# Kernel tuning notes

Hardware: AMD Instinct MI355X
Metric: run time of the kernel (lower is better)

Reference implementation:

```python
import jax, jax.numpy as jnp
import numpy as np

WS = 7          # window size
HN = 6          # heads
C = 192         # emb dim
SHIFT = WS >> 1
L = WS * WS


def _rel_index(ws):
    c = np.stack(np.meshgrid(np.arange(ws), np.arange(ws), indexing='ij'), -1).reshape(-1, 2)
    d = c[:, None, :] - c[None, :, :] + (ws - 1)
    return jnp.asarray(d[..., 0] * (2 * ws - 1) + d[..., 1])  # (L, L) int


def _shift_mask(ws, shift):
    # after intra-window roll by -shift, positions >= ws-shift are wrapped pixels
    r = (np.arange(ws) >= ws - shift).astype(np.int32)
    rid = (2 * r[:, None] + r[None, :]).reshape(-1)  # (L,) region id
    m = np.where(rid[:, None] != rid[None, :], -100.0, 0.0).astype(np.float32)
    return jnp.asarray(m)  # (L, L)


def _ln(x, g, b, eps=1e-5):
    m = jnp.mean(x, -1, keepdims=True)
    v = jnp.mean(jnp.square(x - m), -1, keepdims=True)
    return (x - m) * jax.lax.rsqrt(v + eps) * g + b


def _wmsa(x, qkv_w, qkv_b, proj_w, proj_b, bias_table, rel_idx, mask):
    N, wn, Lx, Cx = x.shape
    dh = Cx // HN
    qkv = x @ qkv_w + qkv_b                      # (N, wn, L, 3C)
    q, k, v = jnp.split(qkv, 3, axis=-1)
    q = q.reshape(N, wn, Lx, HN, dh) * (dh ** -0.5)
    k = k.reshape(N, wn, Lx, HN, dh)
    v = v.reshape(N, wn, Lx, HN, dh)
    a = jnp.einsum('nwqhd,nwkhd->nwhqk', q, k)   # (N, wn, H, L, L)
    a = a + jnp.transpose(bias_table[rel_idx], (2, 0, 1))  # (H, L, L) bias
    if mask is not None:
        a = a + mask                             # (L, L) broadcast
    a = jax.nn.softmax(a, axis=-1)
    o = jnp.einsum('nwhqk,nwkhd->nwqhd', a, v).reshape(N, wn, Lx, Cx)
    return o @ proj_w + proj_b


def _layer(X, g1, b1, g2, b2, qkv_w, qkv_b, proj_w, proj_b, bias_table, rel_idx,
           w1, bb1, w2, bb2, mask):
    tmp = _ln(X, g1, b1)
    tmp = _wmsa(tmp, qkv_w, qkv_b, proj_w, proj_b, bias_table, rel_idx, mask)
    X = _ln(X + tmp, g2, b2)  # drop_path is identity in eval
    h = jax.nn.gelu(X @ w1 + bb1, approximate=False)
    return X + (h @ w2 + bb2)


def setup_inputs() -> dict:
    key = jax.random.key(0)
    ks = jax.random.split(key, 16)
    N, wn = 8, 1024
    s = 0.02
    d = {}
    d['X'] = jax.random.normal(ks[0], (N, wn, L, C), jnp.float32)
    d['ln1_g'] = jnp.ones((C,), jnp.float32)
    d['ln1_b'] = jnp.zeros((C,), jnp.float32)
    d['ln2_g'] = jnp.ones((C,), jnp.float32)
    d['ln2_b'] = jnp.zeros((C,), jnp.float32)
    d['win_qkv_w'] = jax.random.normal(ks[1], (C, 3 * C), jnp.float32) * s
    d['win_qkv_b'] = jnp.zeros((3 * C,), jnp.float32)
    d['win_proj_w'] = jax.random.normal(ks[2], (C, C), jnp.float32) * s
    d['win_proj_b'] = jnp.zeros((C,), jnp.float32)
    d['win_bias'] = jax.random.normal(ks[3], ((2 * WS - 1) ** 2, HN), jnp.float32) * s
    d['swin_qkv_w'] = jax.random.normal(ks[4], (C, 3 * C), jnp.float32) * s
    d['swin_qkv_b'] = jnp.zeros((3 * C,), jnp.float32)
    d['swin_proj_w'] = jax.random.normal(ks[5], (C, C), jnp.float32) * s
    d['swin_proj_b'] = jnp.zeros((C,), jnp.float32)
    d['swin_bias'] = jax.random.normal(ks[6], ((2 * WS - 1) ** 2, HN), jnp.float32) * s
    d['mlp_w1'] = jax.random.normal(ks[7], (C, 4 * C), jnp.float32) * s
    d['mlp_b1'] = jnp.zeros((4 * C,), jnp.float32)
    d['mlp_w2'] = jax.random.normal(ks[8], (4 * C, C), jnp.float32) * s
    d['mlp_b2'] = jnp.zeros((C,), jnp.float32)
    return d


def reference(X, ln1_g, ln1_b, ln2_g, ln2_b,
              win_qkv_w, win_qkv_b, win_proj_w, win_proj_b, win_bias,
              swin_qkv_w, swin_qkv_b, swin_proj_w, swin_proj_b, swin_bias,
              mlp_w1, mlp_b1, mlp_w2, mlp_b2):
    rel_idx = _rel_index(WS)
    mask = _shift_mask(WS, SHIFT)
    N, wn = X.shape[0], X.shape[1]
    # block 1: plain window MSA
    X = _layer(X, ln1_g, ln1_b, ln2_g, ln2_b, win_qkv_w, win_qkv_b, win_proj_w,
               win_proj_b, win_bias, rel_idx, mlp_w1, mlp_b1, mlp_w2, mlp_b2, None)
    # intra-window cyclic shift (torch dims (-2,-3) = W,H axes)
    X = X.reshape(N, wn, WS, WS, C)
    X = jnp.roll(X, (-SHIFT, -SHIFT), axis=(3, 2))
    X = X.reshape(N, wn, L, C)
    # block 2: shifted window MSA with mask
    X = _layer(X, ln1_g, ln1_b, ln2_g, ln2_b, swin_qkv_w, swin_qkv_b, swin_proj_w,
               swin_proj_b, swin_bias, rel_idx, mlp_w1, mlp_b1, mlp_w2, mlp_b2, mask)
    # reverse roll — repo uses dims (-1,-2) = (C, W) axes; replicated faithfully
    X = X.reshape(N, wn, WS, WS, C)
    X = jnp.roll(X, (SHIFT, SHIFT), axis=(4, 3))
    return X.reshape(N, wn, L, C)
```

## Files before the change

kernel.cpp:

```cpp
#include <hip/hip_runtime.h>
#include <hip/hip_bf16.h>
#include <math.h>

#define NTOK 401408
#define NWIN 8192

typedef __attribute__((ext_vector_type(8))) short bf16x8_t;
typedef __attribute__((ext_vector_type(4))) float f32x4_t;

__device__ __forceinline__ float bf2f(unsigned int u) {
    return __uint_as_float(u << 16);
}
__device__ __forceinline__ unsigned short f2bf(float f) {
    unsigned int x = __float_as_uint(f);
    x += 0x7fffu + ((x >> 16) & 1u);
    return (unsigned short)(x >> 16);
}
__device__ __forceinline__ unsigned int pack2bf(float a, float b) {
    return (unsigned int)f2bf(a) | ((unsigned int)f2bf(b) << 16);
}

__global__ void wt_all_kernel(const float* __restrict__ s0, const float* __restrict__ s1,
                              const float* __restrict__ s2, const float* __restrict__ s3,
                              const float* __restrict__ s4, const float* __restrict__ s5,
                              unsigned short* __restrict__ d0, unsigned short* __restrict__ d1,
                              unsigned short* __restrict__ d2, unsigned short* __restrict__ d3,
                              unsigned short* __restrict__ d4, unsigned short* __restrict__ d5) {
    int seg = blockIdx.y;
    const float* W; unsigned short* WT; int K, N;
    switch (seg) {
        case 0:  W = s0; WT = d0; K = 192; N = 576; break;
        case 1:  W = s1; WT = d1; K = 192; N = 576; break;
        case 2:  W = s2; WT = d2; K = 192; N = 192; break;
        case 3:  W = s3; WT = d3; K = 192; N = 192; break;
        case 4:  W = s4; WT = d4; K = 192; N = 768; break;
        default: W = s5; WT = d5; K = 768; N = 192; break;
    }
    int i = blockIdx.x * 256 + threadIdx.x;
    if (i >= N * K) return;
    int n = i / K, k = i - n * K;
    WT[i] = f2bf(W[(size_t)k * N + n]);
}

__global__ void bias_kernel(const float* __restrict__ bt0, const float* __restrict__ bt1,
                            float* __restrict__ bm) {
    int idx = blockIdx.x * 256 + threadIdx.x;
    int variant = blockIdx.y;
    const float* bt = variant ? bt1 : bt0;
    int r = idx & 3, lane = (idx >> 2) & 63, ni = (idx >> 8) & 3, mi = (idx >> 10) & 3, h = idx >> 12;
    int g = lane >> 4;
    int q = ni * 16 + (lane & 15);
    int k = mi * 16 + g * 4 + r;
    float v = 0.f;
    if (q < 49 && k < 49) {
        int qh = q / 7, qw = q - qh * 7, kh = k / 7, kw = k - kh * 7;
        v = bt[((qh - kh + 6) * 13 + (qw - kw + 6)) * 6 + h];
        if (variant) {
            int rq = 2 * (qh >= 4) + (qw >= 4), rk = 2 * (kh >= 4) + (kw >= 4);
            if (rq != rk) v -= 100.f;
        }
    }
    bm[(size_t)variant * 24576 + idx] = v;
}

template<int IN_BF16, int ROLL>
__global__ __launch_bounds__(256) void ln_kernel(const void* __restrict__ in,
                                                 unsigned short* __restrict__ out,
                                                 const float* __restrict__ g,
                                                 const float* __restrict__ b) {
    int tok  = blockIdx.x * 4 + (threadIdx.x >> 6);
    int lane = threadIdx.x & 63;
    int src = tok;
    if (ROLL) {
        int win = tok / 49, p2 = tok - win * 49;
        int h = p2 / 7, w = p2 - h * 7;
        int h2 = h + 3; if (h2 >= 7) h2 -= 7;
        int w2 = w + 3; if (w2 >= 7) w2 -= 7;
        src = win * 49 + h2 * 7 + w2;
    }
    float x0, x1, x2;
    if (IN_BF16) {
        const unsigned short* p = (const unsigned short*)in + (size_t)src * 192;
        x0 = bf2f(p[lane]); x1 = bf2f(p[lane + 64]); x2 = bf2f(p[lane + 128]);
    } else {
        const float* p = (const float*)in + (size_t)src * 192;
        x0 = p[lane]; x1 = p[lane + 64]; x2 = p[lane + 128];
    }
    float s  = x0 + x1 + x2;
    float sq = x0 * x0 + x1 * x1 + x2 * x2;
    for (int o = 32; o; o >>= 1) { s += __shfl_xor(s, o); sq += __shfl_xor(sq, o); }
    float m   = s * (1.f / 192.f);
    float var = sq * (1.f / 192.f) - m * m;
    float r   = rsqrtf(var + 1e-5f);
    unsigned short* q = out + (size_t)tok * 192;
    q[lane]       = f2bf((x0 - m) * r * g[lane]       + b[lane]);
    q[lane + 64]  = f2bf((x1 - m) * r * g[lane + 64]  + b[lane + 64]);
    q[lane + 128] = f2bf((x2 - m) * r * g[lane + 128] + b[lane + 128]);
}

#define EP_QKV        0
#define EP_PROJ1      1
#define EP_PROJ2      2
#define EP_MLP1       3
#define EP_MLP2_TRUNK 4
#define EP_MLP2_OUT   5

template<int NDIM, int KDIM, int NY, int EP>
__global__ __launch_bounds__(256) void gemm_kernel(const unsigned short* __restrict__ A,
                                                   const unsigned short* __restrict__ WT,
                                                   const float* __restrict__ bias,
                                                   const void* __restrict__ res,
                                                   void* __restrict__ out) {
    __shared__ __align__(16) unsigned short As[2][128][40];
    __shared__ __align__(16) unsigned short Bs[2][96][40];
    int tid = threadIdx.x;
    int nwg = gridDim.x;
    int id = blockIdx.x;
    int id2 = (id & 7) * (nwg >> 3) + (id >> 3);
    int by = id2 % NY, bx = id2 / NY;
    int rowBase = bx * 128;
    int colBase = by * 96;

    int cr = tid >> 2, cp = (tid & 3) * 8;
    const unsigned short* Ab = A  + (size_t)rowBase * KDIM + cp;
    const unsigned short* Bb = WT + (size_t)colBase * KDIM + cp;

    uint4 a0, a1, b0, b1;
    const int NT = KDIM / 32;

    #define LOADK(k0)                                                          \
        do {                                                                   \
            a0 = *(const uint4*)(Ab + (size_t)cr * KDIM + (k0));               \
            a1 = *(const uint4*)(Ab + (size_t)(cr + 64) * KDIM + (k0));        \
            b0 = *(const uint4*)(Bb + (size_t)cr * KDIM + (k0));               \
            if (tid < 128) b1 = *(const uint4*)(Bb + (size_t)(cr + 64) * KDIM + (k0)); \
        } while (0)
    #define WRITEK(buf)                                                        \
        do {                                                                   \
            *(uint4*)&As[buf][cr][cp] = a0;                                    \
            *(uint4*)&As[buf][cr + 64][cp] = a1;                               \
            *(uint4*)&Bs[buf][cr][cp] = b0;                                    \
            if (tid < 128) *(uint4*)&Bs[buf][cr + 64][cp] = b1;                \
        } while (0)

    LOADK(0);
    WRITEK(0);

    int wave = tid >> 6, lane = tid & 63;
    int wm = wave >> 1, wn = wave & 1;
    int kq = lane >> 4, lr = lane & 15;

    f32x4_t acc[4][3] = {};
    for (int kt = 0; kt < NT; ++kt) {
        if (kt + 1 < NT) LOADK((kt + 1) * 32);
        __syncthreads();
        int buf = kt & 1;
        bf16x8_t afr[4], bfr[3];
        #pragma unroll
        for (int mi = 0; mi < 4; ++mi)
            afr[mi] = *(const bf16x8_t*)&As[buf][wm * 64 + mi * 16 + lr][kq * 8];
        #pragma unroll
        for (int ni = 0; ni < 3; ++ni)
            bfr[ni] = *(const bf16x8_t*)&Bs[buf][wn * 48 + ni * 16 + lr][kq * 8];
        #pragma unroll
        for (int mi = 0; mi < 4; ++mi)
            #pragma unroll
            for (int ni = 0; ni < 3; ++ni)
                acc[mi][ni] = __builtin_amdgcn_mfma_f32_16x16x32_bf16(
                    afr[mi], bfr[ni], acc[mi][ni], 0, 0, 0);
        if (kt + 1 < NT) WRITEK((kt + 1) & 1);
    }
    #undef LOADK
    #undef WRITEK

    const float* resf = (const float*)res;
    const unsigned short* resb = (const unsigned short*)res;
    #pragma unroll
    for (int mi = 0; mi < 4; ++mi) {
        #pragma unroll
        for (int ni = 0; ni < 3; ++ni) {
            int col = colBase + wn * 48 + ni * 16 + lr;
            float bcol = bias[col];
            #pragma unroll
            for (int r = 0; r < 4; ++r) {
                int rloc = rowBase + wm * 64 + mi * 16 + kq * 4 + r;
                float v = acc[mi][ni][r] + bcol;
                if (EP == EP_QKV) {
                    if (colBase < 192) v *= 0.17677669529663687f;
                    ((unsigned short*)out)[(size_t)rloc * NDIM + col] = f2bf(v);
                } else if (EP == EP_PROJ1) {
                    v += resf[(size_t)rloc * 192 + col];
                    ((unsigned short*)out)[(size_t)rloc * 192 + col] = f2bf(v);
                } else if (EP == EP_PROJ2) {
                    int win = rloc / 49, p2 = rloc - win * 49;
                    int h = p2 / 7, w = p2 - h * 7;
                    int h2 = h + 3; if (h2 >= 7) h2 -= 7;
                    int w2 = w + 3; if (w2 >= 7) w2 -= 7;
                    v += resf[((size_t)win * 49 + h2 * 7 + w2) * 192 + col];
                    ((unsigned short*)out)[(size_t)rloc * 192 + col] = f2bf(v);
                } else if (EP == EP_MLP1) {
                    float gl = 0.5f * v * (1.f + erff(v * 0.70710678118654752f));
                    ((unsigned short*)out)[(size_t)rloc * NDIM + col] = f2bf(gl);
                } else if (EP == EP_MLP2_TRUNK) {
                    v += bf2f((unsigned int)resb[(size_t)rloc * 192 + col]);
                    ((float*)out)[(size_t)rloc * 192 + col] = v;
                } else {
                    v += bf2f((unsigned int)resb[(size_t)rloc * 192 + col]);
                    int win = rloc / 49, p2 = rloc - win * 49;
                    int h = p2 / 7, w = p2 - h * 7;
                    int w2 = w + 3; if (w2 >= 7) w2 -= 7;
                    int c2 = col + 3; if (c2 >= 192) c2 -= 192;
                    ((float*)out)[((size_t)win * 49 + h * 7 + w2) * 192 + c2] = v;
                }
            }
        }
    }
}

__global__ __launch_bounds__(64) void attn_kernel(const unsigned short* __restrict__ qkv,
                                                  const float* __restrict__ bm,
                                                  unsigned short* __restrict__ outp) {
    __shared__ unsigned short P[64][72];
    __shared__ unsigned short VT[32][72];
    int head = blockIdx.x, wloc = blockIdx.y;
    int lane = threadIdx.x;
    int g = lane >> 4, lr = lane & 15;
    const unsigned short* base = qkv + (size_t)wloc * 49 * 576;

    for (int i = lane; i < 256; i += 64) {
        int tok = i >> 2, seg = i & 3;
        uint4 u = make_uint4(0u, 0u, 0u, 0u);
        if (tok < 49)
            u = *(const uint4*)(base + (size_t)tok * 576 + 384 + head * 32 + seg * 8);
        const unsigned short* us = (const unsigned short*)&u;
        #pragma unroll
        for (int j = 0; j < 8; ++j) VT[seg * 8 + j][tok] = us[j];
    }

    bf16x8_t kf[4], qf[4];
    #pragma unroll
    for (int mi = 0; mi < 4; ++mi) {
        int tok = mi * 16 + lr; if (tok > 48) tok = 48;
        kf[mi] = *(const bf16x8_t*)(base + (size_t)tok * 576 + 192 + head * 32 + g * 8);
    }
    #pragma unroll
    for (int ni = 0; ni < 4; ++ni) {
        int tok = ni * 16 + lr; if (tok > 48) tok = 48;
        qf[ni] = *(const bf16x8_t*)(base + (size_t)tok * 576 + head * 32 + g * 8);
    }

    const float* bmh = bm + (size_t)head * 4096;
    f32x4_t acc[4][4];
    #pragma unroll
    for (int mi = 0; mi < 4; ++mi)
        #pragma unroll
        for (int ni = 0; ni < 4; ++ni)
            acc[mi][ni] = *(const f32x4_t*)(bmh + ((mi * 4 + ni) * 64 + lane) * 4);
    #pragma unroll
    for (int mi = 0; mi < 4; ++mi)
        #pragma unroll
        for (int ni = 0; ni < 4; ++ni)
            acc[mi][ni] = __builtin_amdgcn_mfma_f32_16x16x32_bf16(kf[mi], qf[ni], acc[mi][ni], 0, 0, 0);

    float inv[4];
    #pragma unroll
    for (int ni = 0; ni < 4; ++ni) {
        float mx = -1e30f;
        #pragma unroll
        for (int mi = 0; mi < 3; ++mi)
            #pragma unroll
            for (int r = 0; r < 4; ++r) mx = fmaxf(mx, acc[mi][ni][r]);
        mx = fmaxf(mx, (g == 0) ? acc[3][ni][0] : -1e30f);
        mx = fmaxf(mx, __shfl_xor(mx, 16));
        mx = fmaxf(mx, __shfl_xor(mx, 32));
        float p[16], ss = 0.f;
        #pragma unroll
        for (int mi = 0; mi < 3; ++mi)
            #pragma unroll
            for (int r = 0; r < 4; ++r) {
                float e = __expf(acc[mi][ni][r] - mx);
                p[mi * 4 + r] = e; ss += e;
            }
        float e48 = (g == 0) ? __expf(acc[3][ni][0] - mx) : 0.f;
        p[12] = e48; p[13] = p[14] = p[15] = 0.f; ss += e48;
        ss += __shfl_xor(ss, 16);
        ss += __shfl_xor(ss, 32);
        inv[ni] = 1.f / ss;
        int q = ni * 16 + lr;
        #pragma unroll
        for (int mi = 0; mi < 4; ++mi) {
            *(unsigned int*)&P[q][mi * 16 + g * 4]     = pack2bf(p[mi * 4 + 0], p[mi * 4 + 1]);
            *(unsigned int*)&P[q][mi * 16 + g * 4 + 2] = pack2bf(p[mi * 4 + 2], p[mi * 4 + 3]);
        }
    }
    __syncthreads();

    f32x4_t oacc[2][4] = {};
    #pragma unroll
    for (int kt = 0; kt < 2; ++kt) {
        bf16x8_t va[2], pb[4];
        #pragma unroll
        for (int mt = 0; mt < 2; ++mt)
            va[mt] = *(const bf16x8_t*)&VT[mt * 16 + lr][kt * 32 + g * 8];
        #pragma unroll
        for (int nt = 0; nt < 4; ++nt)
            pb[nt] = *(const bf16x8_t*)&P[nt * 16 + lr][kt * 32 + g * 8];
        #pragma unroll
        for (int mt = 0; mt < 2; ++mt)
            #pragma unroll
            for (int nt = 0; nt < 4; ++nt)
                oacc[mt][nt] = __builtin_amdgcn_mfma_f32_16x16x32_bf16(va[mt], pb[nt], oacc[mt][nt], 0, 0, 0);
    }

    #pragma unroll
    for (int nt = 0; nt < 4; ++nt) {
        int q = nt * 16 + lr;
        if (q < 49) {
            size_t tokg = (size_t)wloc * 49 + q;
            unsigned short* op = outp + tokg * 192 + head * 32;
            #pragma unroll
            for (int mt = 0; mt < 2; ++mt) {
                int d0 = mt * 16 + g * 4;
                float a0 = oacc[mt][nt][0] * inv[nt], a1 = oacc[mt][nt][1] * inv[nt];
                float a2 = oacc[mt][nt][2] * inv[nt], a3 = oacc[mt][nt][3] * inv[nt];
                *(unsigned int*)(op + d0)     = pack2bf(a0, a1);
                *(unsigned int*)(op + d0 + 2) = pack2bf(a2, a3);
            }
        }
    }
}

extern "C" void kernel_launch(void* const* d_in, const int* in_sizes, int n_in,
                              void* d_out, int out_size, void* d_ws, size_t ws_size,
                              hipStream_t stream) {
    (void)in_sizes; (void)n_in; (void)out_size; (void)ws_size;
    const float* X     = (const float*)d_in[0];
    const float* ln1_g = (const float*)d_in[1];
    const float* ln1_b = (const float*)d_in[2];
    const float* ln2_g = (const float*)d_in[3];
    const float* ln2_b = (const float*)d_in[4];
    const float* qkv_w[2]  = { (const float*)d_in[5],  (const float*)d_in[10] };
    const float* qkv_b[2]  = { (const float*)d_in[6],  (const float*)d_in[11] };
    const float* proj_w[2] = { (const float*)d_in[7],  (const float*)d_in[12] };
    const float* proj_b[2] = { (const float*)d_in[8],  (const float*)d_in[13] };
    const float* btab[2]   = { (const float*)d_in[9],  (const float*)d_in[14] };
    const float* w1 = (const float*)d_in[15];
    const float* b1 = (const float*)d_in[16];
    const float* w2 = (const float*)d_in[17];
    const float* b2 = (const float*)d_in[18];

    char* p = (char*)d_ws;
    auto takeb = [&](size_t bytes) -> char* {
        char* r = p;
        p += (bytes + 255) & ~(size_t)255;
        return r;
    };
    auto take = [&](size_t elems) -> unsigned short* {
        return (unsigned short*)takeb(elems * 2);
    };
    unsigned short* WTq[2]; unsigned short* WTp[2];
    WTq[0] = take(576 * 192); WTp[0] = take(192 * 192);
    WTq[1] = take(576 * 192); WTp[1] = take(192 * 192);
    unsigned short* WT1 = take(768 * 192);
    unsigned short* WT2 = take(192 * 768);
    float* biasM = (float*)takeb(2 * 24576 * sizeof(float));
    unsigned short* B0 = take((size_t)NTOK * 192);
    unsigned short* X2 = take((size_t)NTOK * 192);
    unsigned short* QH = take((size_t)NTOK * 768);

    wt_all_kernel<<<dim3(576, 6), dim3(256), 0, stream>>>(
        qkv_w[0], qkv_w[1], proj_w[0], proj_w[1], w1, w2,
        WTq[0], WTq[1], WTp[0], WTp[1], WT1, WT2);
    bias_kernel<<<dim3(96, 2), dim3(256), 0, stream>>>(btab[0], btab[1], biasM);

    float* trunk = (float*)d_out;
    const int MB = NTOK / 128;

    for (int blk = 0; blk < 2; ++blk) {
        const float* Xin = (blk == 0) ? X : (const float*)trunk;

        if (blk == 0)
            ln_kernel<0, 0><<<dim3(NTOK / 4), dim3(256), 0, stream>>>((const void*)Xin, B0, ln1_g, ln1_b);
        else
            ln_kernel<0, 1><<<dim3(NTOK / 4), dim3(256), 0, stream>>>((const void*)Xin, B0, ln1_g, ln1_b);

        gemm_kernel<576, 192, 6, EP_QKV><<<dim3(MB * 6), dim3(256), 0, stream>>>(
            B0, WTq[blk], qkv_b[blk], nullptr, (void*)QH);

        attn_kernel<<<dim3(6, NWIN), dim3(64), 0, stream>>>(
            QH, biasM + (size_t)blk * 24576, B0);

        if (blk == 0)
            gemm_kernel<192, 192, 2, EP_PROJ1><<<dim3(MB * 2), dim3(256), 0, stream>>>(
                B0, WTp[blk], proj_b[blk], (const void*)Xin, (void*)X2);
        else
            gemm_kernel<192, 192, 2, EP_PROJ2><<<dim3(MB * 2), dim3(256), 0, stream>>>(
                B0, WTp[blk], proj_b[blk], (const void*)Xin, (void*)X2);

        ln_kernel<1, 0><<<dim3(NTOK / 4), dim3(256), 0, stream>>>((const void*)X2, B0, ln2_g, ln2_b);

        gemm_kernel<768, 192, 8, EP_MLP1><<<dim3(MB * 8), dim3(256), 0, stream>>>(
            B0, WT1, b1, nullptr, (void*)QH);

        if (blk == 0)
            gemm_kernel<192, 768, 2, EP_MLP2_TRUNK><<<dim3(MB * 2), dim3(256), 0, stream>>>(
                QH, WT2, b2, (const void*)B0, (void*)trunk);
        else
            gemm_kernel<192, 768, 2, EP_MLP2_OUT><<<dim3(MB * 2), dim3(256), 0, stream>>>(
                QH, WT2, b2, (const void*)B0, (void*)d_out);
    }
}
```

Measured before the change: 2.957 ms.

## Chunk attention and MLP stages for cache residency and widen GEMM N-tile

```diff
diff --git a/kernel.cpp b/kernel.cpp
--- a/kernel.cpp
+++ b/kernel.cpp
@@ -4,6 +4,9 @@
 
 #define NTOK 401408
 #define NWIN 8192
+#define NCHUNK 4
+#define TOK_PER_CHUNK (NTOK / NCHUNK)
+#define WIN_PER_CHUNK (NWIN / NCHUNK)
 
 typedef __attribute__((ext_vector_type(8))) short bf16x8_t;
 typedef __attribute__((ext_vector_type(4))) float f32x4_t;
@@ -106,41 +109,44 @@
 #define EP_MLP2_OUT   5
 
 template<int NDIM, int KDIM, int NY, int EP>
-__global__ __launch_bounds__(256) void gemm_kernel(const unsigned short* __restrict__ A,
-                                                   const unsigned short* __restrict__ WT,
-                                                   const float* __restrict__ bias,
-                                                   const void* __restrict__ res,
-                                                   void* __restrict__ out) {
+__global__ __launch_bounds__(256, 2) void gemm_kernel(const unsigned short* __restrict__ A,
+                                                      const unsigned short* __restrict__ WT,
+                                                      const float* __restrict__ bias,
+                                                      const void* __restrict__ res,
+                                                      void* __restrict__ out,
+                                                      int row0) {
     __shared__ __align__(16) unsigned short As[2][128][40];
-    __shared__ __align__(16) unsigned short Bs[2][96][40];
+    __shared__ __align__(16) unsigned short Bs[2][192][40];
     int tid = threadIdx.x;
     int nwg = gridDim.x;
     int id = blockIdx.x;
     int id2 = (id & 7) * (nwg >> 3) + (id >> 3);
     int by = id2 % NY, bx = id2 / NY;
     int rowBase = bx * 128;
-    int colBase = by * 96;
+    int colBase = by * 192;
 
     int cr = tid >> 2, cp = (tid & 3) * 8;
     const unsigned short* Ab = A  + (size_t)rowBase * KDIM + cp;
     const unsigned short* Bb = WT + (size_t)colBase * KDIM + cp;
 
-    uint4 a0, a1, b0, b1;
+    uint4 a0, a1, b0, b1, b2;
     const int NT = KDIM / 32;
 
-    #define LOADK(k0)                                                          \
-        do {                                                                   \
-            a0 = *(const uint4*)(Ab + (size_t)cr * KDIM + (k0));               \
-            a1 = *(const uint4*)(Ab + (size_t)(cr + 64) * KDIM + (k0));        \
-            b0 = *(const uint4*)(Bb + (size_t)cr * KDIM + (k0));               \
-            if (tid < 128) b1 = *(const uint4*)(Bb + (size_t)(cr + 64) * KDIM + (k0)); \
+    #define LOADK(k0)                                                               \
+        do {                                                                        \
+            a0 = *(const uint4*)(Ab + (size_t)cr * KDIM + (k0));                    \
+            a1 = *(const uint4*)(Ab + (size_t)(cr + 64) * KDIM + (k0));             \
+            b0 = *(const uint4*)(Bb + (size_t)cr * KDIM + (k0));                    \
+            b1 = *(const uint4*)(Bb + (size_t)(cr + 64) * KDIM + (k0));             \
+            b2 = *(const uint4*)(Bb + (size_t)(cr + 128) * KDIM + (k0));            \
         } while (0)
-    #define WRITEK(buf)                                                        \
-        do {                                                                   \
-            *(uint4*)&As[buf][cr][cp] = a0;                                    \
-            *(uint4*)&As[buf][cr + 64][cp] = a1;                               \
-            *(uint4*)&Bs[buf][cr][cp] = b0;                                    \
-            if (tid < 128) *(uint4*)&Bs[buf][cr + 64][cp] = b1;                \
+    #define WRITEK(buf)                                                             \
+        do {                                                                        \
+            *(uint4*)&As[buf][cr][cp] = a0;                                         \
+            *(uint4*)&As[buf][cr + 64][cp] = a1;                                    \
+            *(uint4*)&Bs[buf][cr][cp] = b0;                                         \
+            *(uint4*)&Bs[buf][cr + 64][cp] = b1;                                    \
+            *(uint4*)&Bs[buf][cr + 128][cp] = b2;                                   \
         } while (0)
 
     LOADK(0);
@@ -150,22 +156,22 @@
     int wm = wave >> 1, wn = wave & 1;
     int kq = lane >> 4, lr = lane & 15;
 
-    f32x4_t acc[4][3] = {};
+    f32x4_t acc[4][6] = {};
     for (int kt = 0; kt < NT; ++kt) {
         if (kt + 1 < NT) LOADK((kt + 1) * 32);
         __syncthreads();
         int buf = kt & 1;
-        bf16x8_t afr[4], bfr[3];
+        bf16x8_t afr[4], bfr[6];
         #pragma unroll
         for (int mi = 0; mi < 4; ++mi)
             afr[mi] = *(const bf16x8_t*)&As[buf][wm * 64 + mi * 16 + lr][kq * 8];
         #pragma unroll
-        for (int ni = 0; ni < 3; ++ni)
-            bfr[ni] = *(const bf16x8_t*)&Bs[buf][wn * 48 + ni * 16 + lr][kq * 8];
+        for (int ni = 0; ni < 6; ++ni)
+            bfr[ni] = *(const bf16x8_t*)&Bs[buf][wn * 96 + ni * 16 + lr][kq * 8];
         #pragma unroll
         for (int mi = 0; mi < 4; ++mi)
             #pragma unroll
-            for (int ni = 0; ni < 3; ++ni)
+            for (int ni = 0; ni < 6; ++ni)
                 acc[mi][ni] = __builtin_amdgcn_mfma_f32_16x16x32_bf16(
                     afr[mi], bfr[ni], acc[mi][ni], 0, 0, 0);
         if (kt + 1 < NT) WRITEK((kt + 1) & 1);
@@ -178,15 +184,15 @@
     #pragma unroll
     for (int mi = 0; mi < 4; ++mi) {
         #pragma unroll
-        for (int ni = 0; ni < 3; ++ni) {
-            int col = colBase + wn * 48 + ni * 16 + lr;
+        for (int ni = 0; ni < 6; ++ni) {
+            int col = colBase + wn * 96 + ni * 16 + lr;
             float bcol = bias[col];
             #pragma unroll
             for (int r = 0; r < 4; ++r) {
                 int rloc = rowBase + wm * 64 + mi * 16 + kq * 4 + r;
                 float v = acc[mi][ni][r] + bcol;
                 if (EP == EP_QKV) {
-                    if (colBase < 192) v *= 0.17677669529663687f;
+                    if (colBase == 0) v *= 0.17677669529663687f;
                     ((unsigned short*)out)[(size_t)rloc * NDIM + col] = f2bf(v);
                 } else if (EP == EP_PROJ1) {
                     v += resf[(size_t)rloc * 192 + col];
@@ -203,10 +209,12 @@
                     ((unsigned short*)out)[(size_t)rloc * NDIM + col] = f2bf(gl);
                 } else if (EP == EP_MLP2_TRUNK) {
                     v += bf2f((unsigned int)resb[(size_t)rloc * 192 + col]);
-                    ((float*)out)[(size_t)rloc * 192 + col] = v;
+                    int grow = row0 + rloc;
+                    ((float*)out)[(size_t)grow * 192 + col] = v;
                 } else {
                     v += bf2f((unsigned int)resb[(size_t)rloc * 192 + col]);
-                    int win = rloc / 49, p2 = rloc - win * 49;
+                    int grow = row0 + rloc;
+                    int win = grow / 49, p2 = grow - win * 49;
                     int h = p2 / 7, w = p2 - h * 7;
                     int w2 = w + 3; if (w2 >= 7) w2 -= 7;
                     int c2 = col + 3; if (c2 >= 192) c2 -= 192;
@@ -219,7 +227,8 @@
 
 __global__ __launch_bounds__(64) void attn_kernel(const unsigned short* __restrict__ qkv,
                                                   const float* __restrict__ bm,
-                                                  unsigned short* __restrict__ outp) {
+                                                  unsigned short* __restrict__ outp,
+                                                  int win0) {
     __shared__ unsigned short P[64][72];
     __shared__ unsigned short VT[32][72];
     int head = blockIdx.x, wloc = blockIdx.y;
@@ -316,7 +325,7 @@
     for (int nt = 0; nt < 4; ++nt) {
         int q = nt * 16 + lr;
         if (q < 49) {
-            size_t tokg = (size_t)wloc * 49 + q;
+            size_t tokg = (size_t)(win0 + wloc) * 49 + q;
             unsigned short* op = outp + tokg * 192 + head * 32;
             #pragma unroll
             for (int mt = 0; mt < 2; ++mt) {
@@ -366,7 +375,8 @@
     float* biasM = (float*)takeb(2 * 24576 * sizeof(float));
     unsigned short* B0 = take((size_t)NTOK * 192);
     unsigned short* X2 = take((size_t)NTOK * 192);
-    unsigned short* QH = take((size_t)NTOK * 768);
+    unsigned short* QC = take((size_t)TOK_PER_CHUNK * 576);
+    unsigned short* HC = take((size_t)TOK_PER_CHUNK * 768);
 
     wt_all_kernel<<<dim3(576, 6), dim3(256), 0, stream>>>(
         qkv_w[0], qkv_w[1], proj_w[0], proj_w[1], w1, w2,
@@ -374,7 +384,7 @@
     bias_kernel<<<dim3(96, 2), dim3(256), 0, stream>>>(btab[0], btab[1], biasM);
 
     float* trunk = (float*)d_out;
-    const int MB = NTOK / 128;
+    const int MBC = TOK_PER_CHUNK / 128;
 
     for (int blk = 0; blk < 2; ++blk) {
         const float* Xin = (blk == 0) ? X : (const float*)trunk;
@@ -384,29 +394,34 @@
         else
             ln_kernel<0, 1><<<dim3(NTOK / 4), dim3(256), 0, stream>>>((const void*)Xin, B0, ln1_g, ln1_b);
 
-        gemm_kernel<576, 192, 6, EP_QKV><<<dim3(MB * 6), dim3(256), 0, stream>>>(
-            B0, WTq[blk], qkv_b[blk], nullptr, (void*)QH);
-
-        attn_kernel<<<dim3(6, NWIN), dim3(64), 0, stream>>>(
-            QH, biasM + (size_t)blk * 24576, B0);
-
-        if (blk == 0)
-            gemm_kernel<192, 192, 2, EP_PROJ1><<<dim3(MB * 2), dim3(256), 0, stream>>>(
-                B0, WTp[blk], proj_b[blk], (const void*)Xin, (void*)X2);
-        else
-            gemm_kernel<192, 192, 2, EP_PROJ2><<<dim3(MB * 2), dim3(256), 0, stream>>>(
-                B0, WTp[blk], proj_b[blk], (const void*)Xin, (void*)X2);
+        for (int c = 0; c < NCHUNK; ++c) {
+            int row0 = c * TOK_PER_CHUNK;
+            gemm_kernel<576, 192, 3, EP_QKV><<<dim3(MBC * 3), dim3(256), 0, stream>>>(
+                B0 + (size_t)row0 * 192, WTq[blk], qkv_b[blk], nullptr, (void*)QC, row0);
+            attn_kernel<<<dim3(6, WIN_PER_CHUNK), dim3(64), 0, stream>>>(
+                QC, biasM + (size_t)blk * 24576, B0, c * WIN_PER_CHUNK);
+            if (blk == 0)
+                gemm_kernel<192, 192, 1, EP_PROJ1><<<dim3(MBC), dim3(256), 0, stream>>>(
+                    B0 + (size_t)row0 * 192, WTp[blk], proj_b[blk],
+                    (const void*)(Xin + (size_t)row0 * 192), (void*)(X2 + (size_t)row0 * 192), row0);
+            else
+                gemm_kernel<192, 192, 1, EP_PROJ2><<<dim3(MBC), dim3(256), 0, stream>>>(
+                    B0 + (size_t)row0 * 192, WTp[blk], proj_b[blk],
+                    (const void*)(Xin + (size_t)row0 * 192), (void*)(X2 + (size_t)row0 * 192), row0);
+        }
 
         ln_kernel<1, 0><<<dim3(NTOK / 4), dim3(256), 0, stream>>>((const void*)X2, B0, ln2_g, ln2_b);
 
-        gemm_kernel<768, 192, 8, EP_MLP1><<<dim3(MB * 8), dim3(256), 0, stream>>>(
-            B0, WT1, b1, nullptr, (void*)QH);
-
-        if (blk == 0)
-            gemm_kernel<192, 768, 2, EP_MLP2_TRUNK><<<dim3(MB * 2), dim3(256), 0, stream>>>(
-                QH, WT2, b2, (const void*)B0, (void*)trunk);
-        else
-            gemm_kernel<192, 768, 2, EP_MLP2_OUT><<<dim3(MB * 2), dim3(256), 0, stream>>>(
-                QH, WT2, b2, (const void*)B0, (void*)d_out);
-    }
-}
+        for (int c = 0; c < NCHUNK; ++c) {
+            int row0 = c * TOK_PER_CHUNK;
+            gemm_kernel<768, 192, 4, EP_MLP1><<<dim3(MBC * 4), dim3(256), 0, stream>>>(
+                B0 + (size_t)row0 * 192, WT1, b1, nullptr, (void*)HC, row0);
+            if (blk == 0)
+                gemm_kernel<192, 768, 1, EP_MLP2_TRUNK><<<dim3(MBC), dim3(256), 0, stream>>>(
+                    HC, WT2, b2, (const void*)(B0 + (size_t)row0 * 192), (void*)trunk, row0);
+            else
+                gemm_kernel<192, 768, 1, EP_MLP2_OUT><<<dim3(MBC), dim3(256), 0, stream>>>(
+                    HC, WT2, b2, (const void*)(B0 + (size_t)row0 * 192), (void*)d_out, row0);
+        }
+    }
+}
```

Measured after the change: 3.025 ms. 2.3% more time.
